# Kernel optimization log

Measured on AMD Instinct MI355X. Metric: run time of the kernel, lower is better.

The kernel has to match this reference:

```python
import jax, jax.numpy as jnp
import numpy as np

N = 16384          # num nodes
E = 524288         # num edges
F_IN = 128         # node_feature_dim
H = 256            # hidden_dim
A = 64             # action_size


def setup_inputs() -> dict:
    key = jax.random.key(0)
    ks = jax.random.split(key, 16)
    def lin(kw, kb, out_d, in_d):
        # kaiming_normal fan_in: std = sqrt(2/in_d); bias zero
        W = jax.random.normal(kw, (out_d, in_d), dtype=jnp.float32) * np.sqrt(2.0 / in_d)
        b = jnp.zeros((out_d,), dtype=jnp.float32)
        return W, b
    node_features = jax.random.normal(ks[0], (N, F_IN), dtype=jnp.float32)
    edge_index = jax.random.randint(ks[1], (2, E), 0, N, dtype=jnp.int64 if jax.config.jax_enable_x64 else jnp.int32)
    W_gnn, b_gnn = lin(ks[2], ks[3], H, F_IN)
    W_a1, b_a1 = lin(ks[4], ks[5], H // 2, H)
    W_a2, b_a2 = lin(ks[6], ks[7], A, H // 2)
    W_c1, b_c1 = lin(ks[8], ks[9], H // 2, H)
    W_c2, b_c2 = lin(ks[10], ks[11], 1, H // 2)
    return {"node_features": node_features, "edge_index": edge_index,
            "W_gnn": W_gnn, "b_gnn": b_gnn,
            "W_a1": W_a1, "b_a1": b_a1, "W_a2": W_a2, "b_a2": b_a2,
            "W_c1": W_c1, "b_c1": b_c1, "W_c2": W_c2, "b_c2": b_c2}


def reference(node_features, edge_index, W_gnn, b_gnn, W_a1, b_a1, W_a2, b_a2,
              W_c1, b_c1, W_c2, b_c2):
    n = node_features.shape[0]
    dt = node_features.dtype
    # dense adjacency build: adj[src, dst] = 1.0 (set, not add), then + I
    adj = jnp.zeros((n, n), dtype=dt).at[edge_index[0], edge_index[1]].set(1.0)
    adj = adj + jnp.eye(n, dtype=dt)
    deg = adj.sum(axis=1, keepdims=True)            # [n,1]
    deg = jnp.where(deg > 0, deg, jnp.ones_like(deg))
    adj = adj / deg                                  # row-normalized
    h = jax.nn.relu(adj @ node_features @ W_gnn.T + b_gnn)  # [n,H]
    g = h.mean(axis=0)                               # [H] graph repr
    a_hidden = jax.nn.relu(g @ W_a1.T + b_a1)
    action_probs = jax.nn.softmax(a_hidden @ W_a2.T + b_a2)  # [A]
    c_hidden = jax.nn.relu(g @ W_c1.T + b_c1)
    value = (c_hidden @ W_c2.T + b_c2)[0]            # scalar
    return action_probs, value
```

## Files before the change

kernel.cpp:

```cpp
#include <hip/hip_runtime.h>
#include <stdint.h>

#define N_NODES 16384
#define E_EDGES 524288
#define F_INF   128
#define H_DIM   256
#define A_DIM   64
#define BCAP    128
#define GBLK    512

#define CNT_OFF    0
#define GACC_OFF   (64 * 1024)
#define DONE_OFF   (65 * 1024)
#define WBF_OFF    (80 * 1024)
#define PART_OFF   (160 * 1024)
#define XBF_OFF    (672 * 1024)
#define BUCKET_OFF (XBF_OFF + (size_t)N_NODES * F_INF * 2)
#define TBF_OFF    (BUCKET_OFF + (size_t)N_NODES * BCAP * 2)

typedef __attribute__((ext_vector_type(8))) short bf16x8;
typedef __attribute__((ext_vector_type(4))) float f32x4;

__device__ __forceinline__ uint32_t f32_to_bf16(float f) {
    uint32_t u = __float_as_uint(f);
    return (u + 0x7FFFu + ((u >> 16) & 1u)) >> 16;
}
__device__ __forceinline__ uint32_t pack_bf16(float lo, float hi) {
    return f32_to_bf16(lo) | (f32_to_bf16(hi) << 16);
}
__device__ __forceinline__ float bf_lo(uint32_t u) { return __uint_as_float(u << 16); }
__device__ __forceinline__ float bf_hi(uint32_t u) { return __uint_as_float(u & 0xFFFF0000u); }

__global__ __launch_bounds__(256) void k_prep(const float* __restrict__ X,
                                              const float* __restrict__ Wg,
                                              uint32_t* __restrict__ Xbf,
                                              uint32_t* __restrict__ Wbf,
                                              uint32_t* __restrict__ cnt,
                                              float* __restrict__ g_acc,
                                              uint32_t* __restrict__ done) {
    int i = blockIdx.x * 256 + threadIdx.x;
    float2 xv = ((const float2*)X)[i];
    Xbf[i] = pack_bf16(xv.x, xv.y);
    if (i < 16384) {
        float2 wv = ((const float2*)Wg)[i];
        Wbf[i] = pack_bf16(wv.x, wv.y);
        cnt[i] = 0u;
    }
    if (i < 256) g_acc[i] = 0.0f;
    if (i == 0) *done = 0u;
}

__global__ __launch_bounds__(256) void k_fill(const int* __restrict__ ei,
                                              uint32_t* __restrict__ cnt,
                                              uint16_t* __restrict__ bucket) {
    int i = blockIdx.x * 256 + threadIdx.x;
    int2 s2 = ((const int2*)ei)[i];
    int2 d2 = ((const int2*)(ei + E_EDGES))[i];
    uint32_t slot0 = atomicAdd(&cnt[s2.x], 1u);
    if (slot0 < BCAP) bucket[(size_t)s2.x * BCAP + slot0] = (uint16_t)d2.x;
    uint32_t slot1 = atomicAdd(&cnt[s2.y], 1u);
    if (slot1 < BCAP) bucket[(size_t)s2.y * BCAP + slot1] = (uint16_t)d2.y;
}

__global__ __launch_bounds__(256) void k_gather(const uint32_t* __restrict__ Xbf,
                                                const uint32_t* __restrict__ cnt,
                                                const uint16_t* __restrict__ bucket,
                                                uint32_t* __restrict__ tbf) {
    __shared__ uint32_t bmp[4][512];
    __shared__ uint16_t q[4][BCAP];
    int wid  = threadIdx.x >> 6;
    int lane = threadIdx.x & 63;
    int n    = blockIdx.x * 4 + wid;
    uint32_t* mybm = bmp[wid];
    uint16_t* myq  = q[wid];

#pragma unroll
    for (int i = 0; i < 8; ++i) mybm[lane + i * 64] = 0u;

    int m = (int)cnt[n];
    if (m > BCAP) m = BCAP;
    const uint16_t* list = bucket + (size_t)n * BCAP;

    int qn = 0;
    for (int base = 0; base < m; base += 64) {
        int idx = base + lane;
        int d = 0;
        bool keep = false;
        if (idx < m) {
            d = list[idx];
            uint32_t bit = 1u << (d & 31);
            uint32_t old = atomicOr(&mybm[d >> 5], bit);
            keep = !(old & bit);
        }
        unsigned long long mask = __ballot(keep);
        int pos = qn + __popcll(mask & ((1ull << lane) - 1ull));
        if (keep) myq[pos] = (uint16_t)d;
        qn += __popcll(mask);
    }

    uint32_t su = Xbf[(size_t)n * 64 + lane];
    float ax = bf_lo(su), ay = bf_hi(su);
    int cdeg = 1 + qn;

    const uint64_t* q8 = (const uint64_t*)myq;
    int i = 0;
    for (; i + 8 <= qn; i += 8) {
        uint64_t p0 = q8[(i >> 2)];
        uint64_t p1 = q8[(i >> 2) + 1];
        int d0 = (int)(p0 & 0xFFFF), d1 = (int)((p0 >> 16) & 0xFFFF);
        int d2 = (int)((p0 >> 32) & 0xFFFF), d3 = (int)(p0 >> 48);
        int d4 = (int)(p1 & 0xFFFF), d5 = (int)((p1 >> 16) & 0xFFFF);
        int d6 = (int)((p1 >> 32) & 0xFFFF), d7 = (int)(p1 >> 48);
        uint32_t u0 = Xbf[(size_t)d0 * 64 + lane];
        uint32_t u1 = Xbf[(size_t)d1 * 64 + lane];
        uint32_t u2 = Xbf[(size_t)d2 * 64 + lane];
        uint32_t u3 = Xbf[(size_t)d3 * 64 + lane];
        uint32_t u4 = Xbf[(size_t)d4 * 64 + lane];
        uint32_t u5 = Xbf[(size_t)d5 * 64 + lane];
        uint32_t u6 = Xbf[(size_t)d6 * 64 + lane];
        uint32_t u7 = Xbf[(size_t)d7 * 64 + lane];
        ax += ((bf_lo(u0) + bf_lo(u1)) + (bf_lo(u2) + bf_lo(u3))) +
              ((bf_lo(u4) + bf_lo(u5)) + (bf_lo(u6) + bf_lo(u7)));
        ay += ((bf_hi(u0) + bf_hi(u1)) + (bf_hi(u2) + bf_hi(u3))) +
              ((bf_hi(u4) + bf_hi(u5)) + (bf_hi(u6) + bf_hi(u7)));
    }
    for (; i < qn; ++i) {
        uint32_t u = Xbf[(size_t)myq[i] * 64 + lane];
        ax += bf_lo(u);
        ay += bf_hi(u);
    }

    float inv = 1.0f / (float)cdeg;
    tbf[(size_t)n * 64 + lane] = pack_bf16(ax * inv, ay * inv);
}

__global__ __launch_bounds__(256) void k_gemm(const uint16_t* __restrict__ Wbf,
                                              const uint16_t* __restrict__ tbf,
                                              const float* __restrict__ bg,
                                              float* __restrict__ part) {
    int wid  = threadIdx.x >> 6;
    int lane = threadIdx.x & 63;
    int j0   = wid * 64;
    int n0   = blockIdx.x * 32;
    int r    = lane & 15;
    int kb   = (lane >> 4) * 8;

    bf16x8 afrag[4][4];
#pragma unroll
    for (int jj = 0; jj < 4; ++jj)
#pragma unroll
        for (int ks = 0; ks < 4; ++ks)
            afrag[jj][ks] = *(const bf16x8*)(Wbf + (size_t)(j0 + jj * 16 + r) * F_INF + ks * 32 + kb);

    float bjv[4][4];
#pragma unroll
    for (int jj = 0; jj < 4; ++jj)
#pragma unroll
        for (int reg = 0; reg < 4; ++reg)
            bjv[jj][reg] = bg[j0 + jj * 16 + ((lane >> 4) << 2) + reg];

    float gp[4][4];
#pragma unroll
    for (int jj = 0; jj < 4; ++jj)
#pragma unroll
        for (int reg = 0; reg < 4; ++reg) gp[jj][reg] = 0.0f;

#pragma unroll
    for (int nt = 0; nt < 2; ++nt) {
        int nb = n0 + nt * 16;
        bf16x8 bfrag[4];
#pragma unroll
        for (int ks = 0; ks < 4; ++ks)
            bfrag[ks] = *(const bf16x8*)(tbf + (size_t)(nb + r) * F_INF + ks * 32 + kb);
#pragma unroll
        for (int jj = 0; jj < 4; ++jj) {
            f32x4 d = {0.0f, 0.0f, 0.0f, 0.0f};
#pragma unroll
            for (int ks = 0; ks < 4; ++ks)
                d = __builtin_amdgcn_mfma_f32_16x16x32_bf16(afrag[jj][ks], bfrag[ks], d, 0, 0, 0);
#pragma unroll
            for (int reg = 0; reg < 4; ++reg)
                gp[jj][reg] += fmaxf(d[reg] + bjv[jj][reg], 0.0f);
        }
    }

    float* prow = part + (size_t)blockIdx.x * H_DIM;
#pragma unroll
    for (int jj = 0; jj < 4; ++jj)
#pragma unroll
        for (int reg = 0; reg < 4; ++reg) {
            float s = gp[jj][reg];
            s += __shfl_xor(s, 1);
            s += __shfl_xor(s, 2);
            s += __shfl_xor(s, 4);
            s += __shfl_xor(s, 8);
            if ((lane & 15) == 0)
                prow[j0 + jj * 16 + ((lane >> 4) << 2) + reg] = s;
        }
}

__global__ __launch_bounds__(256) void k_reduce_heads(
        const float* __restrict__ part, float* __restrict__ g_acc,
        uint32_t* __restrict__ done,
        const float* __restrict__ W_a1, const float* __restrict__ b_a1,
        const float* __restrict__ W_a2, const float* __restrict__ b_a2,
        const float* __restrict__ W_c1, const float* __restrict__ b_c1,
        const float* __restrict__ W_c2, const float* __restrict__ b_c2,
        float* __restrict__ out) {
    __shared__ float gv[H_DIM];
    __shared__ float ah[128];
    __shared__ float ch[128];
    __shared__ uint32_t is_last;
    int tid = threadIdx.x;
    int j   = tid;
    int b0  = blockIdx.x * (GBLK / 16);

    float s = 0.0f;
#pragma unroll 8
    for (int b = 0; b < GBLK / 16; ++b)
        s += part[(size_t)(b0 + b) * H_DIM + j];
    atomicAdd(&g_acc[j], s);

    __threadfence();
    if (tid == 0)
        is_last = (atomicAdd(done, 1u) == 15u);
    __syncthreads();
    if (!is_last) return;

    gv[tid] = __hip_atomic_load(&g_acc[tid], __ATOMIC_ACQUIRE,
                                __HIP_MEMORY_SCOPE_AGENT) * (1.0f / (float)N_NODES);
    __syncthreads();

    if (tid < 128) {
        float acc = b_a1[tid];
        const float* wr = W_a1 + tid * H_DIM;
        for (int k = 0; k < H_DIM; ++k) acc += wr[k] * gv[k];
        ah[tid] = fmaxf(acc, 0.0f);
    } else {
        int i = tid - 128;
        float acc = b_c1[i];
        const float* wr = W_c1 + i * H_DIM;
        for (int k = 0; k < H_DIM; ++k) acc += wr[k] * gv[k];
        ch[i] = fmaxf(acc, 0.0f);
    }
    __syncthreads();

    if (tid < 64) {
        float acc = b_a2[tid];
        const float* wr = W_a2 + tid * 128;
        for (int i = 0; i < 128; ++i) acc += wr[i] * ah[i];
        float m = acc;
        for (int off = 32; off; off >>= 1) m = fmaxf(m, __shfl_xor(m, off));
        float e = expf(acc - m);
        float sm = e;
        for (int off = 32; off; off >>= 1) sm += __shfl_xor(sm, off);
        out[tid] = e / sm;
    } else if (tid < 128) {
        int l = tid - 64;
        float acc = 0.0f;
        for (int i = l; i < 128; i += 64) acc += W_c2[i] * ch[i];
        for (int off = 32; off; off >>= 1) acc += __shfl_xor(acc, off);
        if (l == 0) out[A_DIM] = acc + b_c2[0];
    }
}

extern "C" void kernel_launch(void* const* d_in, const int* in_sizes, int n_in,
                              void* d_out, int out_size, void* d_ws, size_t ws_size,
                              hipStream_t stream) {
    const float* X    = (const float*)d_in[0];
    const int*   ei   = (const int*)d_in[1];
    const float* Wg   = (const float*)d_in[2];
    const float* bg   = (const float*)d_in[3];
    const float* W_a1 = (const float*)d_in[4];
    const float* b_a1 = (const float*)d_in[5];
    const float* W_a2 = (const float*)d_in[6];
    const float* b_a2 = (const float*)d_in[7];
    const float* W_c1 = (const float*)d_in[8];
    const float* b_c1 = (const float*)d_in[9];
    const float* W_c2 = (const float*)d_in[10];
    const float* b_c2 = (const float*)d_in[11];
    float* out = (float*)d_out;

    uint8_t*  ws     = (uint8_t*)d_ws;
    uint32_t* cnt    = (uint32_t*)(ws + CNT_OFF);
    float*    g_acc  = (float*)(ws + GACC_OFF);
    uint32_t* done   = (uint32_t*)(ws + DONE_OFF);
    uint32_t* Wbf32  = (uint32_t*)(ws + WBF_OFF);
    uint16_t* Wbf16  = (uint16_t*)(ws + WBF_OFF);
    float*    part   = (float*)(ws + PART_OFF);
    uint32_t* Xbf    = (uint32_t*)(ws + XBF_OFF);
    uint16_t* bucket = (uint16_t*)(ws + BUCKET_OFF);
    uint32_t* tbf32  = (uint32_t*)(ws + TBF_OFF);
    uint16_t* tbf16  = (uint16_t*)(ws + TBF_OFF);

    k_prep  <<<(N_NODES * F_INF / 2) / 256, 256, 0, stream>>>(X, Wg, Xbf, Wbf32, cnt, g_acc, done);
    k_fill  <<<(E_EDGES / 2) / 256, 256, 0, stream>>>(ei, cnt, bucket);
    k_gather<<<N_NODES / 4, 256, 0, stream>>>(Xbf, cnt, bucket, tbf32);
    k_gemm  <<<GBLK, 256, 0, stream>>>(Wbf16, tbf16, bg, part);
    k_reduce_heads<<<16, 256, 0, stream>>>(part, g_acc, done,
                                           W_a1, b_a1, W_a2, b_a2,
                                           W_c1, b_c1, W_c2, b_c2, out);
}
```

Before: 147.0 us.

## Fuse neighbor gather into GEMM kernel via shared-memory tile

Merges the gather and GEMM kernels. Each wave now aggregates 8 nodes sequentially into a shared-memory bf16 tile, which then feeds the MFMA GEMM directly. This removes the global write and read of the aggregated feature matrix and one kernel launch. The cost is far fewer concurrent waves for the latency-bound gather phase: 512 blocks replace 4096.

```diff
diff --git a/kernel.cpp b/kernel.cpp
--- a/kernel.cpp
+++ b/kernel.cpp
@@ -16,7 +16,6 @@
 #define PART_OFF   (160 * 1024)
 #define XBF_OFF    (672 * 1024)
 #define BUCKET_OFF (XBF_OFF + (size_t)N_NODES * F_INF * 2)
-#define TBF_OFF    (BUCKET_OFF + (size_t)N_NODES * BCAP * 2)
 
 typedef __attribute__((ext_vector_type(8))) short bf16x8;
 typedef __attribute__((ext_vector_type(4))) float f32x4;
@@ -62,96 +61,31 @@
     if (slot1 < BCAP) bucket[(size_t)s2.y * BCAP + slot1] = (uint16_t)d2.y;
 }
 
-__global__ __launch_bounds__(256) void k_gather(const uint32_t* __restrict__ Xbf,
-                                                const uint32_t* __restrict__ cnt,
-                                                const uint16_t* __restrict__ bucket,
-                                                uint32_t* __restrict__ tbf) {
+__global__ __launch_bounds__(256) void k_gather_gemm(
+        const uint32_t* __restrict__ Xbf,
+        const uint32_t* __restrict__ cnt,
+        const uint16_t* __restrict__ bucket,
+        const uint16_t* __restrict__ Wbf,
+        const float* __restrict__ bg,
+        float* __restrict__ part) {
     __shared__ uint32_t bmp[4][512];
     __shared__ uint16_t q[4][BCAP];
+    __shared__ uint32_t tl[32][68];
     int wid  = threadIdx.x >> 6;
     int lane = threadIdx.x & 63;
-    int n    = blockIdx.x * 4 + wid;
     uint32_t* mybm = bmp[wid];
     uint16_t* myq  = q[wid];
-
-#pragma unroll
-    for (int i = 0; i < 8; ++i) mybm[lane + i * 64] = 0u;
-
-    int m = (int)cnt[n];
-    if (m > BCAP) m = BCAP;
-    const uint16_t* list = bucket + (size_t)n * BCAP;
-
-    int qn = 0;
-    for (int base = 0; base < m; base += 64) {
-        int idx = base + lane;
-        int d = 0;
-        bool keep = false;
-        if (idx < m) {
-            d = list[idx];
-            uint32_t bit = 1u << (d & 31);
-            uint32_t old = atomicOr(&mybm[d >> 5], bit);
-            keep = !(old & bit);
-        }
-        unsigned long long mask = __ballot(keep);
-        int pos = qn + __popcll(mask & ((1ull << lane) - 1ull));
-        if (keep) myq[pos] = (uint16_t)d;
-        qn += __popcll(mask);
-    }
-
-    uint32_t su = Xbf[(size_t)n * 64 + lane];
-    float ax = bf_lo(su), ay = bf_hi(su);
-    int cdeg = 1 + qn;
-
-    const uint64_t* q8 = (const uint64_t*)myq;
-    int i = 0;
-    for (; i + 8 <= qn; i += 8) {
-        uint64_t p0 = q8[(i >> 2)];
-        uint64_t p1 = q8[(i >> 2) + 1];
-        int d0 = (int)(p0 & 0xFFFF), d1 = (int)((p0 >> 16) & 0xFFFF);
-        int d2 = (int)((p0 >> 32) & 0xFFFF), d3 = (int)(p0 >> 48);
-        int d4 = (int)(p1 & 0xFFFF), d5 = (int)((p1 >> 16) & 0xFFFF);
-        int d6 = (int)((p1 >> 32) & 0xFFFF), d7 = (int)(p1 >> 48);
-        uint32_t u0 = Xbf[(size_t)d0 * 64 + lane];
-        uint32_t u1 = Xbf[(size_t)d1 * 64 + lane];
-        uint32_t u2 = Xbf[(size_t)d2 * 64 + lane];
-        uint32_t u3 = Xbf[(size_t)d3 * 64 + lane];
-        uint32_t u4 = Xbf[(size_t)d4 * 64 + lane];
-        uint32_t u5 = Xbf[(size_t)d5 * 64 + lane];
-        uint32_t u6 = Xbf[(size_t)d6 * 64 + lane];
-        uint32_t u7 = Xbf[(size_t)d7 * 64 + lane];
-        ax += ((bf_lo(u0) + bf_lo(u1)) + (bf_lo(u2) + bf_lo(u3))) +
-              ((bf_lo(u4) + bf_lo(u5)) + (bf_lo(u6) + bf_lo(u7)));
-        ay += ((bf_hi(u0) + bf_hi(u1)) + (bf_hi(u2) + bf_hi(u3))) +
-              ((bf_hi(u4) + bf_hi(u5)) + (bf_hi(u6) + bf_hi(u7)));
-    }
-    for (; i < qn; ++i) {
-        uint32_t u = Xbf[(size_t)myq[i] * 64 + lane];
-        ax += bf_lo(u);
-        ay += bf_hi(u);
-    }
-
-    float inv = 1.0f / (float)cdeg;
-    tbf[(size_t)n * 64 + lane] = pack_bf16(ax * inv, ay * inv);
-}
-
-__global__ __launch_bounds__(256) void k_gemm(const uint16_t* __restrict__ Wbf,
-                                              const uint16_t* __restrict__ tbf,
-                                              const float* __restrict__ bg,
-                                              float* __restrict__ part) {
-    int wid  = threadIdx.x >> 6;
-    int lane = threadIdx.x & 63;
-    int j0   = wid * 64;
-    int n0   = blockIdx.x * 32;
-    int r    = lane & 15;
-    int kb   = (lane >> 4) * 8;
-
+    int nbase = blockIdx.x * 32;
+
+    int j0 = wid * 64;
+    int r  = lane & 15;
+    int kb = (lane >> 4) * 8;
     bf16x8 afrag[4][4];
 #pragma unroll
     for (int jj = 0; jj < 4; ++jj)
 #pragma unroll
         for (int ks = 0; ks < 4; ++ks)
             afrag[jj][ks] = *(const bf16x8*)(Wbf + (size_t)(j0 + jj * 16 + r) * F_INF + ks * 32 + kb);
-
     float bjv[4][4];
 #pragma unroll
     for (int jj = 0; jj < 4; ++jj)
@@ -159,6 +93,72 @@
         for (int reg = 0; reg < 4; ++reg)
             bjv[jj][reg] = bg[j0 + jj * 16 + ((lane >> 4) << 2) + reg];
 
+    for (int it = 0; it < 8; ++it) {
+        int nl = wid * 8 + it;
+        int n  = nbase + nl;
+
+#pragma unroll
+        for (int i = 0; i < 8; ++i) mybm[lane + i * 64] = 0u;
+
+        int m = (int)cnt[n];
+        if (m > BCAP) m = BCAP;
+        const uint16_t* list = bucket + (size_t)n * BCAP;
+
+        int qn = 0;
+        for (int base = 0; base < m; base += 64) {
+            int idx = base + lane;
+            int d = 0;
+            bool keep = false;
+            if (idx < m) {
+                d = list[idx];
+                uint32_t bit = 1u << (d & 31);
+                uint32_t old = atomicOr(&mybm[d >> 5], bit);
+                keep = !(old & bit);
+            }
+            unsigned long long mask = __ballot(keep);
+            int pos = qn + __popcll(mask & ((1ull << lane) - 1ull));
+            if (keep) myq[pos] = (uint16_t)d;
+            qn += __popcll(mask);
+        }
+
+        uint32_t su = Xbf[(size_t)n * 64 + lane];
+        float ax = bf_lo(su), ay = bf_hi(su);
+        int cdeg = 1 + qn;
+
+        const uint64_t* q8 = (const uint64_t*)myq;
+        int i = 0;
+        for (; i + 8 <= qn; i += 8) {
+            uint64_t p0 = q8[(i >> 2)];
+            uint64_t p1 = q8[(i >> 2) + 1];
+            int d0 = (int)(p0 & 0xFFFF), d1 = (int)((p0 >> 16) & 0xFFFF);
+            int d2 = (int)((p0 >> 32) & 0xFFFF), d3 = (int)(p0 >> 48);
+            int d4 = (int)(p1 & 0xFFFF), d5 = (int)((p1 >> 16) & 0xFFFF);
+            int d6 = (int)((p1 >> 32) & 0xFFFF), d7 = (int)(p1 >> 48);
+            uint32_t u0 = Xbf[(size_t)d0 * 64 + lane];
+            uint32_t u1 = Xbf[(size_t)d1 * 64 + lane];
+            uint32_t u2 = Xbf[(size_t)d2 * 64 + lane];
+            uint32_t u3 = Xbf[(size_t)d3 * 64 + lane];
+            uint32_t u4 = Xbf[(size_t)d4 * 64 + lane];
+            uint32_t u5 = Xbf[(size_t)d5 * 64 + lane];
+            uint32_t u6 = Xbf[(size_t)d6 * 64 + lane];
+            uint32_t u7 = Xbf[(size_t)d7 * 64 + lane];
+            ax += ((bf_lo(u0) + bf_lo(u1)) + (bf_lo(u2) + bf_lo(u3))) +
+                  ((bf_lo(u4) + bf_lo(u5)) + (bf_lo(u6) + bf_lo(u7)));
+            ay += ((bf_hi(u0) + bf_hi(u1)) + (bf_hi(u2) + bf_hi(u3))) +
+                  ((bf_hi(u4) + bf_hi(u5)) + (bf_hi(u6) + bf_hi(u7)));
+        }
+        for (; i < qn; ++i) {
+            uint32_t u = Xbf[(size_t)myq[i] * 64 + lane];
+            ax += bf_lo(u);
+            ay += bf_hi(u);
+        }
+
+        float inv = 1.0f / (float)cdeg;
+        tl[nl][lane] = pack_bf16(ax * inv, ay * inv);
+    }
+
+    __syncthreads();
+
     float gp[4][4];
 #pragma unroll
     for (int jj = 0; jj < 4; ++jj)
@@ -167,11 +167,10 @@
 
 #pragma unroll
     for (int nt = 0; nt < 2; ++nt) {
-        int nb = n0 + nt * 16;
         bf16x8 bfrag[4];
 #pragma unroll
         for (int ks = 0; ks < 4; ++ks)
-            bfrag[ks] = *(const bf16x8*)(tbf + (size_t)(nb + r) * F_INF + ks * 32 + kb);
+            bfrag[ks] = *(const bf16x8*)(&tl[nt * 16 + r][ks * 16 + ((lane >> 4) << 2)]);
 #pragma unroll
         for (int jj = 0; jj < 4; ++jj) {
             f32x4 d = {0.0f, 0.0f, 0.0f, 0.0f};
@@ -212,14 +211,13 @@
     __shared__ float ch[128];
     __shared__ uint32_t is_last;
     int tid = threadIdx.x;
-    int j   = tid;
     int b0  = blockIdx.x * (GBLK / 16);
 
     float s = 0.0f;
 #pragma unroll 8
     for (int b = 0; b < GBLK / 16; ++b)
-        s += part[(size_t)(b0 + b) * H_DIM + j];
-    atomicAdd(&g_acc[j], s);
+        s += part[(size_t)(b0 + b) * H_DIM + tid];
+    atomicAdd(&g_acc[tid], s);
 
     __threadfence();
     if (tid == 0)
@@ -290,13 +288,10 @@
     float*    part   = (float*)(ws + PART_OFF);
     uint32_t* Xbf    = (uint32_t*)(ws + XBF_OFF);
     uint16_t* bucket = (uint16_t*)(ws + BUCKET_OFF);
-    uint32_t* tbf32  = (uint32_t*)(ws + TBF_OFF);
-    uint16_t* tbf16  = (uint16_t*)(ws + TBF_OFF);
 
     k_prep  <<<(N_NODES * F_INF / 2) / 256, 256, 0, stream>>>(X, Wg, Xbf, Wbf32, cnt, g_acc, done);
     k_fill  <<<(E_EDGES / 2) / 256, 256, 0, stream>>>(ei, cnt, bucket);
-    k_gather<<<N_NODES / 4, 256, 0, stream>>>(Xbf, cnt, bucket, tbf32);
-    k_gemm  <<<GBLK, 256, 0, stream>>>(Wbf16, tbf16, bg, part);
+    k_gather_gemm<<<GBLK, 256, 0, stream>>>(Xbf, cnt, bucket, Wbf16, bg, part);
     k_reduce_heads<<<16, 256, 0, stream>>>(part, g_acc, done,
                                            W_a1, b_a1, W_a2, b_a2,
                                            W_c1, b_c1, W_c2, b_c2, out);
```

New measurement: 157.6 us. 7.2% more time.
